# Kernel tuning notes

Hardware: AMD Instinct MI355X
Metric: run time of the kernel (lower is better)

## Reference

```python
import jax, jax.numpy as jnp
import numpy as np

B, H1, H2, D, V1 = 4, 512, 640, 640, 1025  # V1 = vocab_size + 1 (blank)
T, U = 256, 128


def setup_inputs() -> dict:
    key = jax.random.key(0)
    ks = jax.random.split(key, 8)
    s = lambda fan_in: 1.0 / np.sqrt(fan_in)
    return {
        "encoder_outputs": jax.random.normal(ks[0], (B, H1, T), jnp.float32),
        "predictor_outputs": jax.random.normal(ks[1], (B, H2, U), jnp.float32),
        # Linear weights stored as [in, out]
        "W_enc": jax.random.uniform(ks[2], (H1, D), jnp.float32, -s(H1), s(H1)),
        "b_enc": jax.random.uniform(ks[3], (D,), jnp.float32, -s(H1), s(H1)),
        "W_pred": jax.random.uniform(ks[4], (H2, D), jnp.float32, -s(H2), s(H2)),
        "b_pred": jax.random.uniform(ks[5], (D,), jnp.float32, -s(H2), s(H2)),
        "W_out": jax.random.uniform(ks[6], (D, V1), jnp.float32, -s(D), s(D)),
        "b_out": jax.random.uniform(ks[7], (V1,), jnp.float32, -s(D), s(D)),
    }


def reference(encoder_outputs, predictor_outputs, W_enc, b_enc, W_pred, b_pred, W_out, b_out):
    # transpose(1,2): [B,H1,T] -> [B,T,H1], [B,H2,U] -> [B,U,H2], fused into einsum
    f = jnp.einsum("bht,hd->btd", encoder_outputs, W_enc) + b_enc   # [B,T,D]
    g = jnp.einsum("bhu,hd->bud", predictor_outputs, W_pred) + b_pred  # [B,U,D]
    h = jax.nn.relu(f[:, :, None, :] + g[:, None, :, :])            # [B,T,U,D]
    logits = jnp.einsum("btud,dv->btuv", h, W_out) + b_out          # [B,T,U,V+1]
    return jax.nn.log_softmax(logits, axis=-1)
```

## Files before the change

kernel.cpp:

```cpp
#include <hip/hip_runtime.h>
#include <hip/hip_bf16.h>

#define Bb 4
#define Tt 256
#define Uu 128
#define H1 512
#define H2 640
#define Dd 640
#define V1c 1025

typedef __bf16 bf16x8 __attribute__((ext_vector_type(8)));
typedef unsigned short ushort8 __attribute__((ext_vector_type(8)));
typedef unsigned short ushort4v __attribute__((ext_vector_type(4)));
typedef float floatx4 __attribute__((ext_vector_type(4)));

static __device__ __forceinline__ unsigned short f2bf(float x) {
    union { float f; unsigned u; } a; a.f = x;
    unsigned r = a.u + 0x7fffu + ((a.u >> 16) & 1u);
    return (unsigned short)(r >> 16);
}
static __device__ __forceinline__ float bf2f(unsigned short x) {
    union { unsigned u; float f; } a; a.u = ((unsigned)x) << 16; return a.f;
}

__global__ __launch_bounds__(640) void fg_fused(const float* __restrict__ enc,
                                                const float* __restrict__ Wenc,
                                                const float* __restrict__ benc,
                                                float* __restrict__ f,
                                                const float* __restrict__ pred,
                                                const float* __restrict__ Wpred,
                                                const float* __restrict__ bpred,
                                                float* __restrict__ g) {
    __shared__ float s[640 * 8];
    const bool isF = blockIdx.x < 128;
    const float* in   = isF ? enc : pred;
    const float* W    = isF ? Wenc : Wpred;
    const float* bias = isF ? benc : bpred;
    float* out        = isF ? f : g;
    const int H    = isF ? H1 : H2;
    const int Tdim = isF ? Tt : Uu;
    const int blk  = isF ? (int)blockIdx.x : (int)blockIdx.x - 128;
    const int tBlocks = Tdim >> 3;
    const int b  = blk / tBlocks;
    const int t0 = (blk % tBlocks) << 3;
    const float* inB = in + (size_t)b * H * Tdim + t0;
    const int tid = threadIdx.x;

    for (int h = tid; h < H; h += 640) {
        float4 v0 = *(const float4*)(inB + (size_t)h * Tdim);
        float4 v1 = *(const float4*)(inB + (size_t)h * Tdim + 4);
        *(float4*)(&s[h * 8])     = v0;
        *(float4*)(&s[h * 8 + 4]) = v1;
    }
    __syncthreads();

    const int d = tid;
    float acc[8];
    #pragma unroll
    for (int j = 0; j < 8; ++j) acc[j] = 0.f;
    #pragma unroll 4
    for (int h = 0; h < H; ++h) {
        float w = W[(size_t)h * Dd + d];
        float4 s0 = *(const float4*)(&s[h * 8]);
        float4 s1 = *(const float4*)(&s[h * 8 + 4]);
        acc[0] += s0.x * w; acc[1] += s0.y * w; acc[2] += s0.z * w; acc[3] += s0.w * w;
        acc[4] += s1.x * w; acc[5] += s1.y * w; acc[6] += s1.z * w; acc[7] += s1.w * w;
    }
    float bv = bias[d];
    float* o = out + ((size_t)b * Tdim + t0) * Dd + d;
    #pragma unroll
    for (int j = 0; j < 8; ++j) o[(size_t)j * Dd] = acc[j] + bv;
}

__global__ __launch_bounds__(256) void conv_wout2(const float* __restrict__ Wout,
                                                  unsigned short* __restrict__ Wb2,
                                                  float* __restrict__ wtail) {
    __shared__ float tile[32][128];
    const int blk = blockIdx.x;
    const int w = blk / 20;
    const int db = blk % 20;
    const int tid = threadIdx.x;

    #pragma unroll
    for (int i = 0; i < 16; ++i) {
        int idx = tid + 256 * i;
        int d_loc = idx >> 7;
        int v_loc = idx & 127;
        tile[d_loc][v_loc] = Wout[(size_t)(db * 32 + d_loc) * V1c + w * 128 + v_loc];
    }
    __syncthreads();

    #pragma unroll
    for (int k = 0; k < 2; ++k) {
        int gidx = tid * 2 + k;
        int nt  = gidx >> 6;
        int rem = gidx & 63;
        int l15 = rem >> 2;
        int lg  = rem & 3;
        int v_loc = nt * 16 + l15;
        ushort8 pk;
        #pragma unroll
        for (int j = 0; j < 8; ++j) pk[j] = f2bf(tile[lg * 8 + j][v_loc]);
        *(ushort8*)(Wb2 + (size_t)w * 81920 + db * 4096 + gidx * 8) = pk;
    }

    if (blk == 0) {
        for (int dd = tid; dd < Dd; dd += 256) wtail[dd] = Wout[(size_t)dd * V1c + 1024];
    }
}

__global__ __launch_bounds__(512, 2) void joint_main(const float* __restrict__ f,
                                                     const float* __restrict__ g,
                                                     const unsigned short* __restrict__ Wb2,
                                                     const float* __restrict__ wtail,
                                                     const float* __restrict__ b_out,
                                                     float* __restrict__ out) {
    __shared__ __align__(16) union UU {
        unsigned short hlds[2 * 64 * 328];
        float sOut[16 * 1025];
    } u;
    __shared__ float wtld[640];
    __shared__ float sPart[8 * 64];
    __shared__ float sRed[64];
    __shared__ float sTail[64];

    const int tid = threadIdx.x;
    const int l = tid & 63;
    const int w = tid >> 6;
    const int l15 = l & 15;
    const int lg = l >> 4;

    const int blk = blockIdx.x;
    const int uhalf = blk & 1;
    const int t = (blk >> 1) & 255;
    const int b = blk >> 9;
    const int u0 = uhalf * 64;
    const size_t fbase = ((size_t)b * Tt + t) * Dd;
    const size_t gbase = ((size_t)b * Uu + u0) * Dd;
    const size_t rowbase = (size_t)(b * Tt + t) * Uu + u0;

    for (int i = tid; i < Dd; i += 512) wtld[i] = wtail[i];

    floatx4 acc[4][8];
    #pragma unroll
    for (int i = 0; i < 4; ++i)
        #pragma unroll
        for (int j = 0; j < 8; ++j) acc[i][j] = (floatx4){0.f, 0.f, 0.f, 0.f};

    const unsigned short* __restrict__ bbase = Wb2 + (size_t)w * 81920 + (l15 * 32 + lg * 8);
    float tailAcc = 0.f;
    const int srow = w * 8 + (l >> 3);
    const int ssub = l & 7;

    {
        const int row = tid >> 3;
        const float* frow = f + fbase;
        const float* grow = g + gbase + (size_t)row * Dd;
        #pragma unroll
        for (int j = 0; j < 20; ++j) {
            int c4 = (tid & 7) + 8 * j;
            int d = c4 * 4;
            int half = (j >= 10) ? 1 : 0;
            int cloc = c4 - half * 80;
            float4 fv = *(const float4*)(frow + d);
            float4 gv = *(const float4*)(grow + d);
            float h0 = fv.x + gv.x; h0 = h0 > 0.f ? h0 : 0.f;
            float h1 = fv.y + gv.y; h1 = h1 > 0.f ? h1 : 0.f;
            float h2 = fv.z + gv.z; h2 = h2 > 0.f ? h2 : 0.f;
            float h3 = fv.w + gv.w; h3 = h3 > 0.f ? h3 : 0.f;
            ushort4v pk;
            pk.x = f2bf(h0); pk.y = f2bf(h1); pk.z = f2bf(h2); pk.w = f2bf(h3);
            *(ushort4v*)(&u.hlds[half * 20992 + row * 328 + cloc * 4]) = pk;
        }
    }
    __syncthreads();

    {
        ushort8 Bbuf[2][8];
        #pragma unroll
        for (int nt = 0; nt < 8; ++nt)
            Bbuf[0][nt] = *(const ushort8*)(bbase + nt * 512);
        #pragma unroll
        for (int ksg = 0; ksg < 20; ++ksg) {
            if (ksg < 19) {
                #pragma unroll
                for (int nt = 0; nt < 8; ++nt)
                    Bbuf[(ksg + 1) & 1][nt] =
                        *(const ushort8*)(bbase + (ksg + 1) * 4096 + nt * 512);
            }
            const int bufo = (ksg >= 10) ? 20992 : 0;
            const int ks = (ksg >= 10) ? (ksg - 10) : ksg;
            bf16x8 afrag[4];
            #pragma unroll
            for (int mt = 0; mt < 4; ++mt) {
                ushort8 av = *(const ushort8*)(&u.hlds[bufo + (mt * 16 + l15) * 328 + ks * 32 + lg * 8]);
                afrag[mt] = __builtin_bit_cast(bf16x8, av);
            }
            #pragma unroll
            for (int nt = 0; nt < 8; ++nt) {
                bf16x8 bfrag = __builtin_bit_cast(bf16x8, Bbuf[ksg & 1][nt]);
                #pragma unroll
                for (int mt = 0; mt < 4; ++mt) {
                    acc[mt][nt] = __builtin_amdgcn_mfma_f32_16x16x32_bf16(
                        afrag[mt], bfrag, acc[mt][nt], 0, 0, 0);
                }
            }
        }
    }

    #pragma unroll
    for (int j = 0; j < 20; ++j) {
        int c4 = ssub + 8 * j;
        int half = (j >= 10) ? 1 : 0;
        int cloc = c4 - half * 80;
        ushort4v hv = *(const ushort4v*)(&u.hlds[half * 20992 + srow * 328 + cloc * 4]);
        float4 wv = *(const float4*)(&wtld[c4 * 4]);
        tailAcc += bf2f(hv.x) * wv.x + bf2f(hv.y) * wv.y +
                   bf2f(hv.z) * wv.z + bf2f(hv.w) * wv.w;
    }

    tailAcc += __shfl_xor(tailAcc, 1);
    tailAcc += __shfl_xor(tailAcc, 2);
    tailAcc += __shfl_xor(tailAcc, 4);
    if (ssub == 0) sTail[srow] = tailAcc + b_out[1024];

    #pragma unroll
    for (int nt = 0; nt < 8; ++nt) {
        float bo = b_out[w * 128 + nt * 16 + l15];
        #pragma unroll
        for (int mt = 0; mt < 4; ++mt)
            #pragma unroll
            for (int r = 0; r < 4; ++r) acc[mt][nt][r] += bo;
    }

    #pragma unroll
    for (int mt = 0; mt < 4; ++mt) {
        #pragma unroll
        for (int r = 0; r < 4; ++r) {
            float m = acc[mt][0][r];
            #pragma unroll
            for (int nt = 1; nt < 8; ++nt) m = fmaxf(m, acc[mt][nt][r]);
            #pragma unroll
            for (int msk = 1; msk < 16; msk <<= 1) m = fmaxf(m, __shfl_xor(m, msk));
            if (l15 == 0) sPart[w * 64 + mt * 16 + lg * 4 + r] = m;
        }
    }
    __syncthreads();
    if (tid < 64) {
        float m = sTail[tid];
        #pragma unroll
        for (int ww = 0; ww < 8; ++ww) m = fmaxf(m, sPart[ww * 64 + tid]);
        sRed[tid] = m;
    }
    __syncthreads();

    #pragma unroll
    for (int mt = 0; mt < 4; ++mt) {
        #pragma unroll
        for (int r = 0; r < 4; ++r) {
            int row = mt * 16 + lg * 4 + r;
            float mx = sRed[row];
            float sv = 0.f;
            #pragma unroll
            for (int nt = 0; nt < 8; ++nt) sv += __expf(acc[mt][nt][r] - mx);
            #pragma unroll
            for (int msk = 1; msk < 16; msk <<= 1) sv += __shfl_xor(sv, msk);
            if (l15 == 0) sPart[w * 64 + row] = sv;
        }
    }
    __syncthreads();
    if (tid < 64) {
        float mx = sRed[tid];
        float sv = __expf(sTail[tid] - mx);
        #pragma unroll
        for (int ww = 0; ww < 8; ++ww) sv += sPart[ww * 64 + tid];
        sRed[tid] = mx + logf(sv);
    }
    __syncthreads();

    #pragma unroll
    for (int grp = 0; grp < 4; ++grp) {
        #pragma unroll
        for (int nt = 0; nt < 8; ++nt) {
            #pragma unroll
            for (int r = 0; r < 4; ++r) {
                u.sOut[(lg * 4 + r) * 1025 + w * 128 + nt * 16 + l15] =
                    acc[grp][nt][r] - sRed[grp * 16 + lg * 4 + r];
            }
        }
        if (tid < 16) u.sOut[tid * 1025 + 1024] = sTail[grp * 16 + tid] - sRed[grp * 16 + tid];
        __syncthreads();
        float* outp = out + (rowbase + grp * 16) * (size_t)V1c;
        #pragma unroll
        for (int k = 0; k < 8; ++k) {
            int i4 = tid + 512 * k;
            floatx4 v = *(const floatx4*)(&u.sOut[4 * i4]);
            __builtin_nontemporal_store(v, (floatx4*)(outp + 4 * i4));
        }
        if (tid < 4) {
            int i4 = tid + 4096;
            floatx4 v = *(const floatx4*)(&u.sOut[4 * i4]);
            __builtin_nontemporal_store(v, (floatx4*)(outp + 4 * i4));
        }
        __syncthreads();
    }
}

extern "C" void kernel_launch(void* const* d_in, const int* in_sizes, int n_in,
                              void* d_out, int out_size, void* d_ws, size_t ws_size,
                              hipStream_t stream) {
    const float* enc   = (const float*)d_in[0];
    const float* pred  = (const float*)d_in[1];
    const float* Wenc  = (const float*)d_in[2];
    const float* benc  = (const float*)d_in[3];
    const float* Wpred = (const float*)d_in[4];
    const float* bpred = (const float*)d_in[5];
    const float* Wout  = (const float*)d_in[6];
    const float* bout  = (const float*)d_in[7];

    float* f = (float*)d_ws;
    float* g = f + (size_t)Bb * Tt * Dd;
    unsigned short* Wb2 = (unsigned short*)(g + (size_t)Bb * Uu * Dd);
    float* wtail = (float*)(Wb2 + 8 * 81920);

    fg_fused<<<192, 640, 0, stream>>>(enc, Wenc, benc, f, pred, Wpred, bpred, g);
    conv_wout2<<<160, 256, 0, stream>>>(Wout, Wb2, wtail);
    joint_main<<<Bb * Tt * 2, 512, 0, stream>>>(f, g, Wb2, wtail, bout, (float*)d_out);
}
```

Measured before the change: 366.7 us.

## Materialize bf16 joint activations in global memory and stream them into LDS asynchronously

A new h_mat kernel computes relu(f+g) for every (b,t,u) row, converts it to bf16 and writes the full activation tensor to workspace. joint_main then fills its padded LDS tile with direct global-to-LDS 16-byte loads instead of computing the tile with vector ALU work. The aim is to take the add/relu/convert work off the GEMM kernel's critical path and let the LDS fill run asynchronously. The cost is a roughly 167 MB intermediate that must be written and then read back, plus an extra kernel launch, in a kernel already dominated by its large output write.

Result: slower. 438.8 us (+19.7%).

```diff
diff --git a/kernel.cpp b/kernel.cpp
--- a/kernel.cpp
+++ b/kernel.cpp
@@ -21,6 +21,11 @@
 }
 static __device__ __forceinline__ float bf2f(unsigned short x) {
     union { unsigned u; float f; } a; a.u = ((unsigned)x) << 16; return a.f;
+}
+static __device__ __forceinline__ void gload_lds16(const void* gsrc, void* ldst) {
+    __builtin_amdgcn_global_load_lds(
+        (const __attribute__((address_space(1))) void*)gsrc,
+        (__attribute__((address_space(3))) void*)ldst, 16, 0, 0);
 }
 
 __global__ __launch_bounds__(640) void fg_fused(const float* __restrict__ enc,
@@ -109,8 +114,44 @@
     }
 }
 
-__global__ __launch_bounds__(512, 2) void joint_main(const float* __restrict__ f,
-                                                     const float* __restrict__ g,
+__global__ __launch_bounds__(512) void h_mat(const float* __restrict__ f,
+                                             const float* __restrict__ g,
+                                             unsigned short* __restrict__ h) {
+    __shared__ float fr[640];
+    const int blk = blockIdx.x;
+    const int b = blk >> 8;
+    const int t = blk & 255;
+    const int tid = threadIdx.x;
+    if (tid < 160) *(float4*)(&fr[tid * 4]) = *(const float4*)(f + ((size_t)b * Tt + t) * Dd + tid * 4);
+    __syncthreads();
+    const int u = tid >> 2;
+    const int q = tid & 3;
+    const float* grow = g + ((size_t)b * Uu + u) * Dd;
+    unsigned short* hrow = h + ((size_t)(b * Tt + t) * Uu + u) * (size_t)Dd;
+    #pragma unroll 4
+    for (int j = 0; j < 20; ++j) {
+        int o = j * 4 + q;
+        int c0 = o * 8;
+        float4 ga = *(const float4*)(grow + c0);
+        float4 gb = *(const float4*)(grow + c0 + 4);
+        float4 fa = *(const float4*)(&fr[c0]);
+        float4 fb = *(const float4*)(&fr[c0 + 4]);
+        float h0 = fa.x + ga.x; h0 = h0 > 0.f ? h0 : 0.f;
+        float h1 = fa.y + ga.y; h1 = h1 > 0.f ? h1 : 0.f;
+        float h2 = fa.z + ga.z; h2 = h2 > 0.f ? h2 : 0.f;
+        float h3 = fa.w + ga.w; h3 = h3 > 0.f ? h3 : 0.f;
+        float h4 = fb.x + gb.x; h4 = h4 > 0.f ? h4 : 0.f;
+        float h5 = fb.y + gb.y; h5 = h5 > 0.f ? h5 : 0.f;
+        float h6 = fb.z + gb.z; h6 = h6 > 0.f ? h6 : 0.f;
+        float h7 = fb.w + gb.w; h7 = h7 > 0.f ? h7 : 0.f;
+        ushort8 pk;
+        pk[0] = f2bf(h0); pk[1] = f2bf(h1); pk[2] = f2bf(h2); pk[3] = f2bf(h3);
+        pk[4] = f2bf(h4); pk[5] = f2bf(h5); pk[6] = f2bf(h6); pk[7] = f2bf(h7);
+        *(ushort8*)(hrow + c0) = pk;
+    }
+}
+
+__global__ __launch_bounds__(512, 2) void joint_main(const unsigned short* __restrict__ h,
                                                      const unsigned short* __restrict__ Wb2,
                                                      const float* __restrict__ wtail,
                                                      const float* __restrict__ b_out,
@@ -135,10 +176,23 @@
     const int t = (blk >> 1) & 255;
     const int b = blk >> 9;
     const int u0 = uhalf * 64;
-    const size_t fbase = ((size_t)b * Tt + t) * Dd;
-    const size_t gbase = ((size_t)b * Uu + u0) * Dd;
     const size_t rowbase = (size_t)(b * Tt + t) * Uu + u0;
-
+    const unsigned short* hbase = h + rowbase * (size_t)Dd;
+
+    #pragma unroll
+    for (int hh = 0; hh < 2; ++hh) {
+        const unsigned short* hsrc = hbase + hh * 320;
+        #pragma unroll
+        for (int r = 0; r < 6; ++r) {
+            int s = tid + 512 * r;
+            if (s < 2624) {
+                unsigned row = (unsigned)s / 41u;
+                unsigned sir = (unsigned)s - row * 41u;
+                if (sir > 39u) sir = 39u;
+                gload_lds16(hsrc + (size_t)row * Dd + sir * 8, &u.hlds[hh * 20992 + s * 8]);
+            }
+        }
+    }
     for (int i = tid; i < Dd; i += 512) wtld[i] = wtail[i];
 
     floatx4 acc[4][8];
@@ -152,27 +206,6 @@
     const int srow = w * 8 + (l >> 3);
     const int ssub = l & 7;
 
-    {
-        const int row = tid >> 3;
-        const float* frow = f + fbase;
-        const float* grow = g + gbase + (size_t)row * Dd;
-        #pragma unroll
-        for (int j = 0; j < 20; ++j) {
-            int c4 = (tid & 7) + 8 * j;
-            int d = c4 * 4;
-            int half = (j >= 10) ? 1 : 0;
-            int cloc = c4 - half * 80;
-            float4 fv = *(const float4*)(frow + d);
-            float4 gv = *(const float4*)(grow + d);
-            float h0 = fv.x + gv.x; h0 = h0 > 0.f ? h0 : 0.f;
-            float h1 = fv.y + gv.y; h1 = h1 > 0.f ? h1 : 0.f;
-            float h2 = fv.z + gv.z; h2 = h2 > 0.f ? h2 : 0.f;
-            float h3 = fv.w + gv.w; h3 = h3 > 0.f ? h3 : 0.f;
-            ushort4v pk;
-            pk.x = f2bf(h0); pk.y = f2bf(h1); pk.z = f2bf(h2); pk.w = f2bf(h3);
-            *(ushort4v*)(&u.hlds[half * 20992 + row * 328 + cloc * 4]) = pk;
-        }
-    }
     __syncthreads();
 
     {
@@ -322,8 +355,10 @@
     float* g = f + (size_t)Bb * Tt * Dd;
     unsigned short* Wb2 = (unsigned short*)(g + (size_t)Bb * Uu * Dd);
     float* wtail = (float*)(Wb2 + 8 * 81920);
+    unsigned short* h = (unsigned short*)((char*)d_ws + 6ull * 1024 * 1024);
 
     fg_fused<<<192, 640, 0, stream>>>(enc, Wenc, benc, f, pred, Wpred, bpred, g);
     conv_wout2<<<160, 256, 0, stream>>>(Wout, Wb2, wtail);
-    joint_main<<<Bb * Tt * 2, 512, 0, stream>>>(f, g, Wb2, wtail, bout, (float*)d_out);
-}
+    h_mat<<<Bb * Tt, 512, 0, stream>>>(f, g, h);
+    joint_main<<<Bb * Tt * 2, 512, 0, stream>>>(h, Wb2, wtail, bout, (float*)d_out);
+}
```
